# Kernel optimization log

Hardware: AMD Instinct MI355X
Metric: run time of the kernel (lower is better)

## Reference

```python
import jax, jax.numpy as jnp
import numpy as np

B, S, H, L, NH, FF, V, NL = 16, 512, 768, 12, 12, 3072, 30522, 9
DH = H // NH


def setup_inputs() -> dict:
    key = jax.random.key(0)
    ks = iter(jax.random.split(key, 16))
    def w(shape, scale=0.02):
        return jax.random.normal(next(ks), shape, jnp.float32) * scale
    return {
        "input_word_ids": jax.random.randint(next(ks), (B, S), 0, V, jnp.int32),
        "input_mask": jnp.ones((B, S), jnp.int32),
        "input_type_ids": jnp.zeros((B, S), jnp.int32),
        "valid_mask": jax.random.randint(next(ks), (B, S), 0, 2, jnp.int32),
        "word_emb": w((V, H)),
        "pos_emb": w((S, H)),
        "type_emb": w((2, H)),
        "emb_ln_g": jnp.ones((H,), jnp.float32),
        "emb_ln_b": jnp.zeros((H,), jnp.float32),
        "Wq": w((L, H, H)), "bq": jnp.zeros((L, H), jnp.float32),
        "Wk": w((L, H, H)), "bk": jnp.zeros((L, H), jnp.float32),
        "Wv": w((L, H, H)), "bv": jnp.zeros((L, H), jnp.float32),
        "Wo": w((L, H, H)), "bo": jnp.zeros((L, H), jnp.float32),
        "ln1_g": jnp.ones((L, H), jnp.float32), "ln1_b": jnp.zeros((L, H), jnp.float32),
        "W1": w((L, H, FF)), "b1": jnp.zeros((L, FF), jnp.float32),
        "W2": w((L, FF, H)), "b2": jnp.zeros((L, H), jnp.float32),
        "ln2_g": jnp.ones((L, H), jnp.float32), "ln2_b": jnp.zeros((L, H), jnp.float32),
        "cls_W": w((H, NL)), "cls_b": jnp.zeros((NL,), jnp.float32),
    }


def _layer_norm(x, g, b):
    m = x.mean(-1, keepdims=True)
    v = ((x - m) ** 2).mean(-1, keepdims=True)
    return (x - m) * jax.lax.rsqrt(v + 1e-12) * g + b


def reference(input_word_ids, input_mask, input_type_ids, valid_mask,
              word_emb, pos_emb, type_emb, emb_ln_g, emb_ln_b,
              Wq, bq, Wk, bk, Wv, bv, Wo, bo, ln1_g, ln1_b,
              W1, b1, W2, b2, ln2_g, ln2_b, cls_W, cls_b):
    b, s = input_word_ids.shape
    # --- BERT embeddings ---
    x = word_emb[input_word_ids] + pos_emb[None, :s] + type_emb[input_type_ids]
    x = _layer_norm(x, emb_ln_g, emb_ln_b)  # [B,S,H]
    attn_bias = (1.0 - input_mask.astype(jnp.float32))[:, None, None, :] * -1e9
    scale = 1.0 / np.sqrt(DH).astype(np.float32)

    def step(h, p):
        wq, bq_, wk, bk_, wv, bv_, wo, bo_, g1, gb1, w1, wb1, w2, wb2, g2, gb2 = p
        q = (h @ wq + bq_).reshape(b, s, NH, DH)
        k = (h @ wk + bk_).reshape(b, s, NH, DH)
        v = (h @ wv + bv_).reshape(b, s, NH, DH)
        scores = jnp.einsum('bqhd,bkhd->bhqk', q, k) * scale + attn_bias
        probs = jax.nn.softmax(scores, axis=-1)
        ctx = jnp.einsum('bhqk,bkhd->bqhd', probs, v).reshape(b, s, H)
        h = _layer_norm(h + ctx @ wo + bo_, g1, gb1)
        ff = jax.nn.gelu(h @ w1 + wb1, approximate=False)
        h = _layer_norm(h + ff @ w2 + wb2, g2, gb2)
        return h, None

    params = (Wq, bq, Wk, bk, Wv, bv, Wo, bo, ln1_g, ln1_b, W1, b1, W2, b2, ln2_g, ln2_b)
    x, _ = jax.lax.scan(step, x, params)

    # --- valid-token compaction (vectorized form of the python double loop) ---
    # valid tokens packed to the front (stable order), remainder zero-padded
    invalid = (1 - valid_mask).astype(jnp.int32)
    perm = jnp.argsort(invalid, axis=1, stable=True)          # [B,S]
    compact = jnp.take_along_axis(x, perm[:, :, None], axis=1)
    counts = valid_mask.sum(axis=1)                           # [B]
    keep = (jnp.arange(s)[None, :] < counts[:, None])[:, :, None]
    compact = jnp.where(keep, compact, jnp.zeros((), x.dtype))
    # dropout is identity at inference (training=False)
    logits = jax.nn.softmax(compact @ cls_W + cls_b, axis=-1)  # [B,S,NL]
    return logits
```

## Files before the change

kernel.cpp:

```cpp
#include <hip/hip_runtime.h>
#include <cstdint>
#include <cstddef>

#define B_ 16
#define S_ 512
#define H_ 768
#define L_ 12
#define NH_ 12
#define DH_ 64
#define FF_ 3072
#define NL_ 9
#define QKV_ 2304

typedef _Float16 f16x8 __attribute__((ext_vector_type(8)));
typedef float f32x4 __attribute__((ext_vector_type(4)));

__device__ __forceinline__ void load_lds16(const void* g, void* l) {
  __builtin_amdgcn_global_load_lds(
      (const __attribute__((address_space(1))) unsigned int*)g,
      (__attribute__((address_space(3))) unsigned int*)l, 16, 0, 0);
}

__device__ __forceinline__ float block_sum256(float v, float* red) {
#pragma unroll
  for (int off = 32; off; off >>= 1) v += __shfl_down(v, off);
  __syncthreads();
  if ((threadIdx.x & 63) == 0) red[threadIdx.x >> 6] = v;
  __syncthreads();
  return red[0] + red[1] + red[2] + red[3];
}

__device__ __forceinline__ float gelu_f(float x) {
  return 0.5f * x * (1.0f + erff(x * 0.70710678118654752f));
}

__global__ __launch_bounds__(256) void embed_ln_kernel(
    const int* __restrict__ wid, const int* __restrict__ tpid,
    const float* __restrict__ we, const float* __restrict__ pe,
    const float* __restrict__ te, const float* __restrict__ g,
    const float* __restrict__ bb, float* __restrict__ h,
    _Float16* __restrict__ hb) {
  __shared__ float red[4];
  int tok = blockIdx.x;
  int s = tok & (S_ - 1);
  int w = wid[tok], tp = tpid[tok];
  int t = threadIdx.x;
  float x[3];
#pragma unroll
  for (int i = 0; i < 3; ++i) {
    int j = t + i * 256;
    x[i] = we[(size_t)w * H_ + j] + pe[(size_t)s * H_ + j] + te[(size_t)tp * H_ + j];
  }
  float m = block_sum256(x[0] + x[1] + x[2], red) * (1.0f / H_);
  float d0 = x[0] - m, d1 = x[1] - m, d2 = x[2] - m;
  float var = block_sum256(d0 * d0 + d1 * d1 + d2 * d2, red) * (1.0f / H_);
  float rs = rsqrtf(var + 1e-12f);
#pragma unroll
  for (int i = 0; i < 3; ++i) {
    int j = t + i * 256;
    float v = (x[i] - m) * rs * g[j] + bb[j];
    h[(size_t)tok * H_ + j] = v;
    hb[(size_t)tok * H_ + j] = (_Float16)v;
  }
}

__global__ __launch_bounds__(256) void add_ln_kernel(
    float* __restrict__ h, const float* __restrict__ delta,
    const float* __restrict__ g, const float* __restrict__ bb,
    _Float16* __restrict__ hb) {
  __shared__ float red[4];
  int tok = blockIdx.x;
  int t = threadIdx.x;
  float x[3];
#pragma unroll
  for (int i = 0; i < 3; ++i) {
    int j = t + i * 256;
    x[i] = h[(size_t)tok * H_ + j] + delta[(size_t)tok * H_ + j];
  }
  float m = block_sum256(x[0] + x[1] + x[2], red) * (1.0f / H_);
  float d0 = x[0] - m, d1 = x[1] - m, d2 = x[2] - m;
  float var = block_sum256(d0 * d0 + d1 * d1 + d2 * d2, red) * (1.0f / H_);
  float rs = rsqrtf(var + 1e-12f);
#pragma unroll
  for (int i = 0; i < 3; ++i) {
    int j = t + i * 256;
    float v = (x[i] - m) * rs * g[j] + bb[j];
    h[(size_t)tok * H_ + j] = v;
    hb[(size_t)tok * H_ + j] = (_Float16)v;
  }
}

__global__ __launch_bounds__(256) void convert_weights_kernel(
    const float* __restrict__ Wq, const float* __restrict__ Wk,
    const float* __restrict__ Wv, const float* __restrict__ Wo,
    const float* __restrict__ W1, const float* __restrict__ W2,
    _Float16* __restrict__ qT, _Float16* __restrict__ kT,
    _Float16* __restrict__ vT, _Float16* __restrict__ oT,
    _Float16* __restrict__ w1T, _Float16* __restrict__ w2T) {
  __shared__ float T[64][65];
  int id = blockIdx.x;
  const float* src;
  _Float16* dst;
  int K, N, tk, tn;
  if (id < 576) {
    int mat = id / 144, t = id % 144;
    K = 768; N = 768; tk = t / 12; tn = t % 12;
    src = (mat == 0) ? Wq : (mat == 1) ? Wk : (mat == 2) ? Wv : Wo;
    dst = (mat == 0) ? qT : (mat == 1) ? kT : (mat == 2) ? vT : oT;
  } else if (id < 1152) {
    int t = id - 576; K = 768; N = 3072; tk = t / 48; tn = t % 48;
    src = W1; dst = w1T;
  } else {
    int t = id - 1152; K = 3072; N = 768; tk = t / 12; tn = t % 12;
    src = W2; dst = w2T;
  }
  int tid = threadIdx.x;
  int k0 = tk * 64, n0 = tn * 64;
  {
    int r = tid >> 4, c4 = (tid & 15) * 4;
#pragma unroll
    for (int i = 0; i < 4; ++i) {
      float4 v = *(const float4*)&src[(size_t)(k0 + r + i * 16) * N + n0 + c4];
      T[r + i * 16][c4 + 0] = v.x;
      T[r + i * 16][c4 + 1] = v.y;
      T[r + i * 16][c4 + 2] = v.z;
      T[r + i * 16][c4 + 3] = v.w;
    }
  }
  __syncthreads();
#pragma unroll
  for (int i = 0; i < 2; ++i) {
    int chunk = tid + i * 256;
    int n = chunk >> 3, kc = (chunk & 7) * 8;
    f16x8 o;
#pragma unroll
    for (int j = 0; j < 8; ++j) o[j] = (_Float16)T[kc + j][n];
    *(f16x8*)&dst[(size_t)(n0 + n) * K + k0 + kc] = o;
  }
}

__global__ void biascat_kernel(const float* __restrict__ bq, const float* __restrict__ bk,
                               const float* __restrict__ bv, float* __restrict__ o) {
  int t = threadIdx.x;
  for (int j = t; j < H_; j += 256) {
    o[j] = bq[j];
    o[H_ + j] = bk[j];
    o[2 * H_ + j] = bv[j];
  }
}

template <int OUT>
__global__ __launch_bounds__(256) void gemm_f16(
    const _Float16* __restrict__ A, const _Float16* __restrict__ Bt,
    const float* __restrict__ bias, void* __restrict__ Cv,
    int M, int N, int K) {
  __shared__ _Float16 As[128 * 32];
  __shared__ _Float16 Bs[128 * 32];
  int tid = threadIdx.x;
  int lane = tid & 63, w = tid >> 6;
  int wr = w >> 1, wc = w & 1;
  int row0 = blockIdx.y * 128, col0 = blockIdx.x * 128;
  int l15 = lane & 15, kb = lane >> 4;

  int srow = lane >> 2, scol = (lane & 3) * 8;
  const _Float16* gA0 = A + (size_t)(row0 + (w * 2 + 0) * 16 + srow) * K + scol;
  const _Float16* gA1 = A + (size_t)(row0 + (w * 2 + 1) * 16 + srow) * K + scol;
  const _Float16* gB0 = Bt + (size_t)(col0 + (w * 2 + 0) * 16 + srow) * K + scol;
  const _Float16* gB1 = Bt + (size_t)(col0 + (w * 2 + 1) * 16 + srow) * K + scol;
  char* lA0 = (char*)As + (w * 2 + 0) * 1024;
  char* lA1 = (char*)As + (w * 2 + 1) * 1024;
  char* lB0 = (char*)Bs + (w * 2 + 0) * 1024;
  char* lB1 = (char*)Bs + (w * 2 + 1) * 1024;

  f32x4 acc[4][4] = {};
  int nk = K >> 5;
  for (int kt = 0; kt < nk; ++kt) {
    int ko = kt * 32;
    __syncthreads();
    load_lds16(gA0 + ko, lA0);
    load_lds16(gA1 + ko, lA1);
    load_lds16(gB0 + ko, lB0);
    load_lds16(gB1 + ko, lB1);
    __syncthreads();
    f16x8 af[4], bf[4];
#pragma unroll
    for (int m = 0; m < 4; ++m)
      af[m] = *(const f16x8*)&As[(wr * 64 + m * 16 + l15) * 32 + kb * 8];
#pragma unroll
    for (int n = 0; n < 4; ++n)
      bf[n] = *(const f16x8*)&Bs[(wc * 64 + n * 16 + l15) * 32 + kb * 8];
#pragma unroll
    for (int m = 0; m < 4; ++m)
#pragma unroll
      for (int n = 0; n < 4; ++n)
        acc[m][n] = __builtin_amdgcn_mfma_f32_16x16x32_f16(af[m], bf[n], acc[m][n], 0, 0, 0);
  }
#pragma unroll
  for (int n = 0; n < 4; ++n) {
    int col = col0 + wc * 64 + n * 16 + l15;
    float bv = bias[col];
#pragma unroll
    for (int m = 0; m < 4; ++m) {
      int rowb = row0 + wr * 64 + m * 16 + kb * 4;
#pragma unroll
      for (int r = 0; r < 4; ++r) {
        float v = acc[m][n][r] + bv;
        if (OUT == 2) v = gelu_f(v);
        if (OUT == 0)
          ((float*)Cv)[(size_t)(rowb + r) * N + col] = v;
        else
          ((_Float16*)Cv)[(size_t)(rowb + r) * N + col] = (_Float16)v;
      }
    }
  }
}

__global__ __launch_bounds__(256) void vtrans_kernel(
    const _Float16* __restrict__ v, int RS, _Float16* __restrict__ vt) {
  __shared__ _Float16 T[64][72];
  int s0 = blockIdx.x * 64;
  int bh = blockIdx.y;
  int b = bh / NH_, h = bh % NH_;
  int tid = threadIdx.x;
#pragma unroll
  for (int i = 0; i < 2; ++i) {
    int chunk = tid + i * 256;
    int s = chunk >> 3, dc = (chunk & 7) * 8;
    *(f16x8*)&T[s][dc] = *(const f16x8*)&v[(size_t)(b * S_ + s0 + s) * RS + h * DH_ + dc];
  }
  __syncthreads();
#pragma unroll
  for (int i = 0; i < 2; ++i) {
    int chunk = tid + i * 256;
    int d = chunk >> 3, sc = (chunk & 7) * 8;
    f16x8 o;
#pragma unroll
    for (int j = 0; j < 8; ++j) o[j] = T[sc + j][d];
    *(f16x8*)&vt[(size_t)(bh * DH_ + d) * S_ + s0 + sc] = o;
  }
}

__global__ __launch_bounds__(256) void flash_attn_kernel(
    const _Float16* __restrict__ q, const _Float16* __restrict__ k,
    const _Float16* __restrict__ vt, int RS, const int* __restrict__ mask,
    _Float16* __restrict__ ctx) {
  __shared__ _Float16 Ks[128 * 72];
  __shared__ _Float16 Vs[64 * 136];
  __shared__ _Float16 Ps[4][16 * 136];
  __shared__ float biasz[S_];
  int qt = blockIdx.x, h = blockIdx.y, b = blockIdx.z;
  int tid = threadIdx.x, lane = tid & 63, w = tid >> 6;
  int l15 = lane & 15, kb = lane >> 4;
  const float C = 0.125f * 1.44269504088896f;

  for (int i = tid; i < S_; i += 256)
    biasz[i] = (1.0f - (float)mask[b * S_ + i]) * (-1e9f * C);

  int qrow = b * S_ + qt * 64 + w * 16 + l15;
  f16x8 qf[2];
  qf[0] = *(const f16x8*)&q[(size_t)qrow * RS + h * DH_ + kb * 8];
  qf[1] = *(const f16x8*)&q[(size_t)qrow * RS + h * DH_ + 32 + kb * 8];

  auto loadKV = [&](int kt, f16x8* rk, f16x8* rv) {
#pragma unroll
    for (int i = 0; i < 4; ++i) {
      int idx = tid + i * 256;
      int r = idx >> 3, c = idx & 7;
      rk[i] = *(const f16x8*)&k[(size_t)(b * S_ + kt * 128 + r) * RS + h * DH_ + c * 8];
      int d = idx >> 4, c2 = idx & 15;
      rv[i] = *(const f16x8*)&vt[(size_t)((b * NH_ + h) * DH_ + d) * S_ + kt * 128 + c2 * 8];
    }
  };

  float m_run[4], l_run[4];
  f32x4 o[4] = {};
#pragma unroll
  for (int r = 0; r < 4; ++r) { m_run[r] = -1e30f; l_run[r] = 0.f; }

  f16x8 rk[4], rv[4];
  loadKV(0, rk, rv);
  for (int kt = 0; kt < 4; ++kt) {
    __syncthreads();
#pragma unroll
    for (int i = 0; i < 4; ++i) {
      int idx = tid + i * 256;
      int r = idx >> 3, c = idx & 7;
      *(f16x8*)&Ks[r * 72 + c * 8] = rk[i];
      int d = idx >> 4, c2 = idx & 15;
      *(f16x8*)&Vs[d * 136 + c2 * 8] = rv[i];
    }
    __syncthreads();
    if (kt < 3) loadKV(kt + 1, rk, rv);
    f32x4 s[8];
#pragma unroll
    for (int nf = 0; nf < 8; ++nf) {
      f16x8 b0 = *(const f16x8*)&Ks[(nf * 16 + l15) * 72 + kb * 8];
      f16x8 b1 = *(const f16x8*)&Ks[(nf * 16 + l15) * 72 + 32 + kb * 8];
      f32x4 z = {};
      z = __builtin_amdgcn_mfma_f32_16x16x32_f16(qf[0], b0, z, 0, 0, 0);
      z = __builtin_amdgcn_mfma_f32_16x16x32_f16(qf[1], b1, z, 0, 0, 0);
      s[nf] = z;
    }
    float zb[8];
#pragma unroll
    for (int nf = 0; nf < 8; ++nf) zb[nf] = biasz[kt * 128 + nf * 16 + l15];
    float pw[8][4];
    float corr[4];
#pragma unroll
    for (int r = 0; r < 4; ++r) {
      float mx = -1e30f;
#pragma unroll
      for (int nf = 0; nf < 8; ++nf) mx = fmaxf(mx, s[nf][r] * C + zb[nf]);
#pragma unroll
      for (int d = 1; d < 16; d <<= 1) mx = fmaxf(mx, __shfl_xor(mx, d));
      float mnew = fmaxf(m_run[r], mx);
      float cr = exp2f(m_run[r] - mnew);
      m_run[r] = mnew;
      corr[r] = cr;
      float sum = 0.f;
#pragma unroll
      for (int nf = 0; nf < 8; ++nf) {
        float pv = exp2f(s[nf][r] * C + zb[nf] - mnew);
        pw[nf][r] = pv;
        sum += pv;
      }
#pragma unroll
      for (int d = 1; d < 16; d <<= 1) sum += __shfl_xor(sum, d);
      l_run[r] = l_run[r] * cr + sum;
    }
#pragma unroll
    for (int nf2 = 0; nf2 < 4; ++nf2)
#pragma unroll
      for (int r = 0; r < 4; ++r) o[nf2][r] *= corr[r];
#pragma unroll
    for (int nf = 0; nf < 8; ++nf)
#pragma unroll
      for (int r = 0; r < 4; ++r)
        Ps[w][(kb * 4 + r) * 136 + nf * 16 + l15] = (_Float16)pw[nf][r];
#pragma unroll
    for (int ks = 0; ks < 4; ++ks) {
      f16x8 pa = *(const f16x8*)&Ps[w][l15 * 136 + ks * 32 + kb * 8];
#pragma unroll
      for (int nf2 = 0; nf2 < 4; ++nf2) {
        f16x8 vb2 = *(const f16x8*)&Vs[(nf2 * 16 + l15) * 136 + ks * 32 + kb * 8];
        o[nf2] = __builtin_amdgcn_mfma_f32_16x16x32_f16(pa, vb2, o[nf2], 0, 0, 0);
      }
    }
  }
  float inv[4];
#pragma unroll
  for (int r = 0; r < 4; ++r) inv[r] = 1.0f / fmaxf(l_run[r], 1e-37f);
#pragma unroll
  for (int nf2 = 0; nf2 < 4; ++nf2)
#pragma unroll
    for (int r = 0; r < 4; ++r) {
      int row = b * S_ + qt * 64 + w * 16 + kb * 4 + r;
      ctx[(size_t)row * H_ + h * DH_ + nf2 * 16 + l15] = (_Float16)(o[nf2][r] * inv[r]);
    }
}

__global__ void compact_idx_kernel(const int* __restrict__ valid, int* __restrict__ dest) {
  int b = threadIdx.x;
  if (b >= B_) return;
  int cnt = 0;
  for (int s = 0; s < S_; ++s) {
    int vv = valid[b * S_ + s];
    dest[b * S_ + s] = vv ? cnt : -1;
    cnt += vv;
  }
}

__global__ __launch_bounds__(256) void scatter_kernel(
    const float* __restrict__ h, const int* __restrict__ dest,
    float* __restrict__ compact) {
  int tok = blockIdx.x;
  int d = dest[tok];
  if (d < 0) return;
  int b = tok >> 9;
  size_t src = (size_t)tok * H_;
  size_t dst = ((size_t)(b * S_ + d)) * H_;
  for (int j = threadIdx.x; j < H_; j += 256) compact[dst + j] = h[src + j];
}

__global__ __launch_bounds__(256) void cls_kernel(
    const float* __restrict__ x, const float* __restrict__ W,
    const float* __restrict__ bias2, float* __restrict__ out) {
  int lane = threadIdx.x & 63, wv = threadIdx.x >> 6;
  int tok = blockIdx.x * 4 + wv;
  float acc[NL_] = {};
  for (int hh = lane; hh < H_; hh += 64) {
    float xv = x[(size_t)tok * H_ + hh];
#pragma unroll
    for (int n = 0; n < NL_; ++n) acc[n] = fmaf(xv, W[hh * NL_ + n], acc[n]);
  }
#pragma unroll
  for (int n = 0; n < NL_; ++n) {
#pragma unroll
    for (int off = 32; off; off >>= 1) acc[n] += __shfl_down(acc[n], off);
  }
  if (lane == 0) {
    float vls[NL_], mx = -1e30f;
#pragma unroll
    for (int n = 0; n < NL_; ++n) {
      vls[n] = acc[n] + bias2[n];
      mx = fmaxf(mx, vls[n]);
    }
    float s = 0.f;
#pragma unroll
    for (int n = 0; n < NL_; ++n) {
      vls[n] = expf(vls[n] - mx);
      s += vls[n];
    }
    float inv = 1.0f / s;
#pragma unroll
    for (int n = 0; n < NL_; ++n) out[(size_t)tok * NL_ + n] = vls[n] * inv;
  }
}

extern "C" void kernel_launch(void* const* d_in, const int* in_sizes, int n_in,
                              void* d_out, int out_size, void* d_ws, size_t ws_size,
                              hipStream_t stream) {
  const int* wid = (const int*)d_in[0];
  const int* mask = (const int*)d_in[1];
  const int* tpid = (const int*)d_in[2];
  const int* valid = (const int*)d_in[3];
  const float* we = (const float*)d_in[4];
  const float* pe = (const float*)d_in[5];
  const float* te = (const float*)d_in[6];
  const float* eg = (const float*)d_in[7];
  const float* eb = (const float*)d_in[8];
  const float* Wq = (const float*)d_in[9];
  const float* bq = (const float*)d_in[10];
  const float* Wk = (const float*)d_in[11];
  const float* bk = (const float*)d_in[12];
  const float* Wv = (const float*)d_in[13];
  const float* bv = (const float*)d_in[14];
  const float* Wo = (const float*)d_in[15];
  const float* bo = (const float*)d_in[16];
  const float* g1 = (const float*)d_in[17];
  const float* gb1 = (const float*)d_in[18];
  const float* W1 = (const float*)d_in[19];
  const float* bf1 = (const float*)d_in[20];
  const float* W2 = (const float*)d_in[21];
  const float* bf2 = (const float*)d_in[22];
  const float* g2 = (const float*)d_in[23];
  const float* gb2 = (const float*)d_in[24];
  const float* cW = (const float*)d_in[25];
  const float* cb = (const float*)d_in[26];
  float* out = (float*)d_out;

  const size_t TOK = (size_t)B_ * S_;
  char* ws = (char*)d_ws;
  float* h = (float*)ws;
  _Float16* hb = (_Float16*)(ws + 25165824);
  float* t1 = (float*)(ws + 37748736);
  char* un1 = ws + 62914560;
  _Float16* qkv = (_Float16*)un1;
  _Float16* vt = (_Float16*)(un1 + 37748736);
  _Float16* ffh = (_Float16*)un1;
  _Float16* ctx = (_Float16*)(ws + 113246208);
  char* wbuf = ws + 125829120;
  _Float16* wqT = (_Float16*)wbuf;
  _Float16* wkT = (_Float16*)(wbuf + 1179648);
  _Float16* wvT = (_Float16*)(wbuf + 2359296);
  _Float16* woT = (_Float16*)(wbuf + 3538944);
  _Float16* w1T = (_Float16*)(wbuf + 4718592);
  _Float16* w2T = (_Float16*)(wbuf + 9437184);
  int* dest = (int*)(ws + 139984896);
  float* qkvb = (float*)(ws + 140017664);

  dim3 blk(256);
  embed_ln_kernel<<<dim3((unsigned)TOK), blk, 0, stream>>>(wid, tpid, we, pe, te, eg, eb, h, hb);

  dim3 gQKV(QKV_ / 128, TOK / 128);
  dim3 gH(H_ / 128, TOK / 128);
  dim3 gF(FF_ / 128, TOK / 128);
  for (int l = 0; l < L_; ++l) {
    convert_weights_kernel<<<dim3(1728), blk, 0, stream>>>(
        Wq + (size_t)l * H_ * H_, Wk + (size_t)l * H_ * H_,
        Wv + (size_t)l * H_ * H_, Wo + (size_t)l * H_ * H_,
        W1 + (size_t)l * H_ * FF_, W2 + (size_t)l * FF_ * H_,
        wqT, wkT, wvT, woT, w1T, w2T);
    biascat_kernel<<<dim3(1), blk, 0, stream>>>(bq + l * H_, bk + l * H_, bv + l * H_, qkvb);
    gemm_f16<1><<<gQKV, blk, 0, stream>>>(hb, wqT, qkvb, qkv, (int)TOK, QKV_, H_);
    vtrans_kernel<<<dim3(S_ / 64, B_ * NH_), blk, 0, stream>>>(qkv + 2 * H_, QKV_, vt);
    flash_attn_kernel<<<dim3(S_ / 64, NH_, B_), blk, 0, stream>>>(
        qkv, qkv + H_, vt, QKV_, mask, ctx);
    gemm_f16<0><<<gH, blk, 0, stream>>>(ctx, woT, bo + l * H_, t1, (int)TOK, H_, H_);
    add_ln_kernel<<<dim3((unsigned)TOK), blk, 0, stream>>>(h, t1, g1 + l * H_, gb1 + l * H_, hb);
    gemm_f16<2><<<gF, blk, 0, stream>>>(hb, w1T, bf1 + l * FF_, ffh, (int)TOK, FF_, H_);
    gemm_f16<0><<<gH, blk, 0, stream>>>(ffh, w2T, bf2 + l * H_, t1, (int)TOK, H_, FF_);
    add_ln_kernel<<<dim3((unsigned)TOK), blk, 0, stream>>>(h, t1, g2 + l * H_, gb2 + l * H_, hb);
  }

  compact_idx_kernel<<<1, 64, 0, stream>>>(valid, dest);
  hipMemsetAsync(t1, 0, TOK * H_ * sizeof(float), stream);
  scatter_kernel<<<dim3((unsigned)TOK), blk, 0, stream>>>(h, dest, t1);
  cls_kernel<<<dim3((unsigned)(TOK / 4)), blk, 0, stream>>>(t1, cW, cb, out);
}
```

Before: 4.107 ms.

## Double-buffer LDS tiles in f16 GEMM and swizzle workgroup order

The GEMM now keeps two LDS buffers for the A and B tiles and issues the global-to-LDS loads for the next k-step before computing on the current one. This removes one barrier per iteration and lets memory latency overlap with MFMA work. A remapping of workgroup IDs in groups of eight is also added, intended to improve L2 reuse across neighbouring tiles. The cost is twice the LDS per block, which can lower occupancy, and there is a risk that the single barrier does not order the async LDS writes correctly.

```diff
diff --git a/kernel.cpp b/kernel.cpp
--- a/kernel.cpp
+++ b/kernel.cpp
@@ -154,46 +154,64 @@
     const _Float16* __restrict__ A, const _Float16* __restrict__ Bt,
     const float* __restrict__ bias, void* __restrict__ Cv,
     int M, int N, int K) {
-  __shared__ _Float16 As[128 * 32];
-  __shared__ _Float16 Bs[128 * 32];
+  __shared__ _Float16 As[2][128 * 32];
+  __shared__ _Float16 Bs[2][128 * 32];
   int tid = threadIdx.x;
   int lane = tid & 63, w = tid >> 6;
   int wr = w >> 1, wc = w & 1;
-  int row0 = blockIdx.y * 128, col0 = blockIdx.x * 128;
   int l15 = lane & 15, kb = lane >> 4;
+
+  int nwg = gridDim.x * gridDim.y;
+  int bid = blockIdx.y * gridDim.x + blockIdx.x;
+  int swz = bid;
+  if ((nwg & 7) == 0) {
+    int cpx = nwg >> 3;
+    swz = (bid & 7) * cpx + (bid >> 3);
+  }
+  int bx = swz % gridDim.x, by = swz / gridDim.x;
+  int row0 = by * 128, col0 = bx * 128;
 
   int srow = lane >> 2, scol = (lane & 3) * 8;
   const _Float16* gA0 = A + (size_t)(row0 + (w * 2 + 0) * 16 + srow) * K + scol;
   const _Float16* gA1 = A + (size_t)(row0 + (w * 2 + 1) * 16 + srow) * K + scol;
   const _Float16* gB0 = Bt + (size_t)(col0 + (w * 2 + 0) * 16 + srow) * K + scol;
   const _Float16* gB1 = Bt + (size_t)(col0 + (w * 2 + 1) * 16 + srow) * K + scol;
-  char* lA0 = (char*)As + (w * 2 + 0) * 1024;
-  char* lA1 = (char*)As + (w * 2 + 1) * 1024;
-  char* lB0 = (char*)Bs + (w * 2 + 0) * 1024;
-  char* lB1 = (char*)Bs + (w * 2 + 1) * 1024;
+  int o0 = (w * 2 + 0) * 1024;
+  int o1 = (w * 2 + 1) * 1024;
 
   f32x4 acc[4][4] = {};
   int nk = K >> 5;
+
+  {
+    load_lds16(gA0, (char*)&As[0][0] + o0);
+    load_lds16(gA1, (char*)&As[0][0] + o1);
+    load_lds16(gB0, (char*)&Bs[0][0] + o0);
+    load_lds16(gB1, (char*)&Bs[0][0] + o1);
+  }
+  __syncthreads();
+
   for (int kt = 0; kt < nk; ++kt) {
-    int ko = kt * 32;
-    __syncthreads();
-    load_lds16(gA0 + ko, lA0);
-    load_lds16(gA1 + ko, lA1);
-    load_lds16(gB0 + ko, lB0);
-    load_lds16(gB1 + ko, lB1);
-    __syncthreads();
+    int cur = kt & 1;
+    if (kt + 1 < nk) {
+      int ko = (kt + 1) * 32;
+      load_lds16(gA0 + ko, (char*)&As[cur ^ 1][0] + o0);
+      load_lds16(gA1 + ko, (char*)&As[cur ^ 1][0] + o1);
+      load_lds16(gB0 + ko, (char*)&Bs[cur ^ 1][0] + o0);
+      load_lds16(gB1 + ko, (char*)&Bs[cur ^ 1][0] + o1);
+    }
     f16x8 af[4], bf[4];
 #pragma unroll
     for (int m = 0; m < 4; ++m)
-      af[m] = *(const f16x8*)&As[(wr * 64 + m * 16 + l15) * 32 + kb * 8];
+      af[m] = *(const f16x8*)&As[cur][(wr * 64 + m * 16 + l15) * 32 + kb * 8];
 #pragma unroll
     for (int n = 0; n < 4; ++n)
-      bf[n] = *(const f16x8*)&Bs[(wc * 64 + n * 16 + l15) * 32 + kb * 8];
+      bf[n] = *(const f16x8*)&Bs[cur][(wc * 64 + n * 16 + l15) * 32 + kb * 8];
 #pragma unroll
     for (int m = 0; m < 4; ++m)
 #pragma unroll
       for (int n = 0; n < 4; ++n)
         acc[m][n] = __builtin_amdgcn_mfma_f32_16x16x32_f16(af[m], bf[n], acc[m][n], 0, 0, 0);
+    __syncthreads();
   }
 #pragma unroll
   for (int n = 0; n < 4; ++n) {
```

Measured after the change: 3.693 ms. -10.1%, faster.
